# Kernel optimization log

Measured on AMD Instinct MI355X. Metric: run time of the kernel, lower is better.

Reference implementation:

```python
import jax, jax.numpy as jnp
import numpy as np

DIM = 768
HID = 1536
EPS = 1e-12
SCALE = float(np.sqrt(DIM))


def _layernorm(x, gamma, beta):
    mu = jnp.mean(x, axis=-1, keepdims=True)
    var = jnp.mean(jnp.square(x - mu), axis=-1, keepdims=True)
    return (x - mu) * jax.lax.rsqrt(var + EPS) * gamma + beta


def setup_inputs() -> dict:
    key = jax.random.key(0)
    ks = jax.random.split(key, 16)
    s = 1.0 / np.sqrt(DIM)
    sh = 1.0 / np.sqrt(HID)
    x = jax.random.normal(ks[0], (8, 2048, DIM), dtype=jnp.float32)
    return {
        "x": x,
        "Wq": jax.random.uniform(ks[1], (DIM, DIM), jnp.float32, -s, s),
        "bq": jax.random.uniform(ks[2], (DIM,), jnp.float32, -s, s),
        "Wk": jax.random.uniform(ks[3], (DIM, DIM), jnp.float32, -s, s),
        "bk": jax.random.uniform(ks[4], (DIM,), jnp.float32, -s, s),
        "Wv": jax.random.uniform(ks[5], (DIM, DIM), jnp.float32, -s, s),
        "bv": jax.random.uniform(ks[6], (DIM,), jnp.float32, -s, s),
        "Wp": jax.random.uniform(ks[7], (DIM, DIM), jnp.float32, -s, s),
        "bp": jax.random.uniform(ks[8], (DIM,), jnp.float32, -s, s),
        "g1": jnp.ones((DIM,), jnp.float32),
        "be1": jnp.zeros((DIM,), jnp.float32),
        "W1": jax.random.uniform(ks[9], (HID, DIM), jnp.float32, -s, s),
        "b1": jax.random.uniform(ks[10], (HID,), jnp.float32, -s, s),
        "W2": jax.random.uniform(ks[11], (DIM, HID), jnp.float32, -sh, sh),
        "b2": jax.random.uniform(ks[12], (DIM,), jnp.float32, -sh, sh),
        "g2": jnp.ones((DIM,), jnp.float32),
        "be2": jnp.zeros((DIM,), jnp.float32),
    }


def reference(x, Wq, bq, Wk, bk, Wv, bv, Wp, bp, g1, be1, W1, b1, W2, b2, g2, be2):
    # NOTE: original code does NOT split into heads; single full-dim bmm attention.
    Q = jnp.einsum("bsd,ed->bse", x, Wq) + bq  # [B,S,D]
    K = jnp.einsum("bsd,ed->bse", x, Wk) + bk
    V = jnp.einsum("bsd,ed->bse", x, Wv) + bv
    alpha = jnp.einsum("bqd,bkd->bqk", Q, K) / SCALE  # [B,S,S]
    alpha = jax.nn.softmax(alpha, axis=-1)
    attn = jnp.einsum("bqk,bkd->bqd", alpha, V)
    attn = jnp.einsum("bsd,ed->bse", attn, Wp) + bp  # linear_proj
    h = _layernorm(x + attn, g1, be1)
    mlp = jax.nn.gelu(jnp.einsum("bsd,hd->bsh", h, W1) + b1, approximate=False)
    mlp = jnp.einsum("bsh,dh->bsd", mlp, W2) + b2
    return _layernorm(h + mlp, g2, be2)
```

## Files before the change

kernel.cpp:

```cpp
#include <hip/hip_runtime.h>
#include <math.h>

#define D_MODEL 768
#define D_HID   1536
#define N_BATCH 8
#define SEQLEN  2048
#define NROWS   (N_BATCH*SEQLEN)

typedef unsigned short u16;
typedef unsigned char  u8;
typedef __attribute__((ext_vector_type(8))) short bfrag;
typedef __attribute__((ext_vector_type(4))) float facc;

__device__ __forceinline__ u16 f2bf(float f) {
  unsigned u = __float_as_uint(f);
  u += 0x7fffu + ((u >> 16) & 1u);
  return (u16)(u >> 16);
}
__device__ __forceinline__ float bf2f(u16 u) {
  return __uint_as_float((unsigned)u << 16);
}
__device__ __forceinline__ u8 f2fp8(float f) {
  return (u8)(__builtin_amdgcn_cvt_pk_fp8_f32(f, f, 0, 0) & 0xff);
}

__device__ __forceinline__ void async16(const void* g, void* l) {
  __builtin_amdgcn_global_load_lds((const __attribute__((address_space(1))) void*)g,
                                   (__attribute__((address_space(3))) void*)l,
                                   16, 0, 0);
}
__device__ __forceinline__ void wg_barrier() {
  asm volatile("" ::: "memory");
  __builtin_amdgcn_s_barrier();
  asm volatile("" ::: "memory");
}
#define VMCNT(n) asm volatile("s_waitcnt vmcnt(" #n ")" ::: "memory")

__global__ __launch_bounds__(256) void cvt_all(
    const float* __restrict__ x,  const float* __restrict__ Wq,
    const float* __restrict__ Wk, const float* __restrict__ Wv,
    const float* __restrict__ Wp, const float* __restrict__ W1,
    const float* __restrict__ W2, const float* __restrict__ bq,
    const float* __restrict__ bk, const float* __restrict__ bv,
    u16* __restrict__ XB, u16* __restrict__ WQKV, u16* __restrict__ WPB,
    u16* __restrict__ W1B, u16* __restrict__ W2B, float* __restrict__ BQKV,
    float* __restrict__ LSUM) {
  long i = (long)blockIdx.x * 256 + threadIdx.x;
  const float* src; u16* dst; long off;
  if      (i < 3145728) { src = x;  dst = XB;             off = i; }
  else if (i < 3293184) { src = Wq; dst = WQKV;           off = i - 3145728; }
  else if (i < 3440640) { src = Wk; dst = WQKV + 589824;  off = i - 3293184; }
  else if (i < 3588096) { src = Wv; dst = WQKV + 1179648; off = i - 3440640; }
  else if (i < 3735552) { src = Wp; dst = WPB;            off = i - 3588096; }
  else if (i < 4030464) { src = W1; dst = W1B;            off = i - 3735552; }
  else if (i < 4325376) { src = W2; dst = W2B;            off = i - 4030464; }
  else if (i < 4325952) {
    long j = i - 4325376;
    const float* s = (j < 192) ? bq : (j < 384) ? bk : bv;
    long o = (j < 192) ? j : (j < 384) ? j - 192 : j - 384;
    ((float4*)BQKV)[j] = ((const float4*)s)[o];
    return;
  } else if (i < 4330048) {
    float4 zz = {0.f, 0.f, 0.f, 0.f};
    ((float4*)LSUM)[i - 4325952] = zz;
    return;
  } else return;
  float4 v = ((const float4*)src)[off];
  ushort4 o4;
  o4.x = f2bf(v.x); o4.y = f2bf(v.y); o4.z = f2bf(v.z); o4.w = f2bf(v.w);
  *reinterpret_cast<ushort4*>(dst + off * 4) = o4;
}

enum { EPI_EXP = 1, EPI_DIV = 2, EPI_GELU = 4, EPI_QKV = 5, EPI_RES = 6 };

template<int EPI>
__global__ __launch_bounds__(256, 3)
void gemm_bt(const u16* __restrict__ Aall, const u16* __restrict__ Ball,
             void* __restrict__ Cout,
             int M, int N, int K,
             long sA, long sB, long sC,
             const float* __restrict__ bias,
             const u16* __restrict__ resid,
             float* __restrict__ lsum,
             float scale)
{
  __shared__ __align__(16) char smem[49152];
  const int z = blockIdx.z;
  const u16* A = Aall + (long)z * sA;
  const u16* B = Ball + (long)z * sB;
  const int bm = blockIdx.x, bn = blockIdx.y;
  const int tid = (int)threadIdx.x;
  const int lane = tid & 63, wv = tid >> 6;
  const int wr = wv >> 1, wc = wv & 1;

  facc acc[4][4] = {};

  const int srow2 = tid >> 2;
  const int c4 = tid & 3;
  const int skey = (srow2 >> 1) & 3;
  const int sc = ((c4 ^ skey) << 3);
  const u16* Abase = A + (long)(bm * 128) * K;
  const u16* Bbase = B + (long)(bn * 128) * K;
  const int fr = lane & 15, g0 = lane >> 4;
  const int rkey = (fr >> 1) & 3;
  const int nt = K >> 5;

  auto STAGE = [&](int t, int b) {
    char* Asb = smem + b * 16384;
    char* Bsb = Asb + 8192;
    const long k0 = (long)t << 5;
#pragma unroll
    for (int p = 0; p < 2; ++p) {
      async16(Abase + (long)(p * 64 + srow2) * K + k0 + sc, Asb + p * 4096 + tid * 16);
      async16(Bbase + (long)(p * 64 + srow2) * K + k0 + sc, Bsb + p * 4096 + tid * 16);
    }
  };

  STAGE(0, 0); STAGE(1, 1);
  int rb_ = 0, sb_ = 2;
  for (int t = 0; t < nt; ++t) {
    if (t < nt - 1) { VMCNT(4); } else { VMCNT(0); }
    wg_barrier();
    if (t + 2 < nt) STAGE(t + 2, sb_);
    const u16* As = (const u16*)(smem + rb_ * 16384);
    const u16* Bs = As + 4096;
    bfrag af[4], bf[4];
#pragma unroll
    for (int i = 0; i < 4; ++i) {
      const int r = wr * 64 + i * 16 + fr;
      af[i] = *(const bfrag*)(As + r * 32 + ((g0 ^ rkey) << 3));
    }
#pragma unroll
    for (int j = 0; j < 4; ++j) {
      const int r = wc * 64 + j * 16 + fr;
      bf[j] = *(const bfrag*)(Bs + r * 32 + ((g0 ^ rkey) << 3));
    }
    __builtin_amdgcn_s_setprio(1);
#pragma unroll
    for (int i = 0; i < 4; ++i)
#pragma unroll
      for (int j = 0; j < 4; ++j)
        acc[i][j] = __builtin_amdgcn_mfma_f32_16x16x32_bf16(af[i], bf[j], acc[i][j], 0, 0, 0);
    __builtin_amdgcn_s_setprio(0);
    rb_ = (rb_ == 2) ? 0 : rb_ + 1;
    sb_ = (sb_ == 2) ? 0 : sb_ + 1;
  }
  wg_barrier();

  const int rb = bm * 128 + wr * 64;
  const int cb = bn * 128 + wc * 64;
  const int quad = lane >> 4;

  if constexpr (EPI == EPI_QKV) {
    const int c64 = bn * 2 + wc;
    const int which = c64 / 12;
    float bj[4];
#pragma unroll
    for (int j = 0; j < 4; ++j) bj[j] = bias[cb + j * 16 + fr];
    if (which == 2) {
      u8* VT_ = (u8*)resid;
      const int zb = rb >> 11;
      const int seqb = (rb & 2047) + quad * 4;
      const int dimb = (c64 - 24) * 64;
#pragma unroll
      for (int i = 0; i < 4; ++i) {
#pragma unroll
        for (int j = 0; j < 4; ++j) {
          const int dim = dimb + j * 16 + fr;
          unsigned v01 = __builtin_amdgcn_cvt_pk_fp8_f32(acc[i][j][0] + bj[j],
                                                         acc[i][j][1] + bj[j], 0, 0);
          unsigned v23 = __builtin_amdgcn_cvt_pk_fp8_f32(acc[i][j][2] + bj[j],
                                                         acc[i][j][3] + bj[j], 0, 0);
          unsigned w = (v01 & 0xffffu) | (v23 << 16);
          *reinterpret_cast<unsigned*>(VT_ + (long)zb * D_MODEL * SEQLEN +
                                       (long)dim * SEQLEN + seqb + i * 16) = w;
        }
      }
      return;
    }
    u8* ep8 = (u8*)(smem + wv * 8192);
    u8* Cg = (u8*)Cout + (long)which * NROWS * D_MODEL;
    const int cbo = (c64 - which * 12) * 64;
#pragma unroll
    for (int i = 0; i < 4; ++i)
#pragma unroll
      for (int r = 0; r < 4; ++r) {
        const int lrow = i * 16 + quad * 4 + r;
#pragma unroll
        for (int j = 0; j < 4; ++j)
          ep8[lrow * 64 + j * 16 + fr] = f2fp8(acc[i][j][r] + bj[j]);
      }
#pragma unroll
    for (int it = 0; it < 4; ++it) {
      const int lr = it * 16 + (lane >> 2);
      const int ch = (lane & 3) << 4;
      int4 d = *(const int4*)(ep8 + lr * 64 + ch);
      *reinterpret_cast<int4*>(Cg + (long)(rb + lr) * D_MODEL + cbo + ch) = d;
    }
  } else if constexpr (EPI == EPI_GELU) {
    u16* ep16 = (u16*)(smem + wv * 8192);
    u16* Cg = (u16*)Cout + (long)z * sC;
    float bj[4];
#pragma unroll
    for (int j = 0; j < 4; ++j) bj[j] = bias[cb + j * 16 + fr];
#pragma unroll
    for (int i = 0; i < 4; ++i) {
#pragma unroll
      for (int r = 0; r < 4; ++r) {
        const int lrow = i * 16 + quad * 4 + r;
#pragma unroll
        for (int j = 0; j < 4; ++j) {
          float t = acc[i][j][r] + bj[j];
          float y = 0.7978845608f * (t + 0.044715f * t * t * t);
          float e = __expf(-2.f * fabsf(y));
          float th = (1.f - e) / (1.f + e);
          th = (y < 0.f) ? -th : th;
          ep16[lrow * 64 + j * 16 + fr] = f2bf(0.5f * t * (1.f + th));
        }
      }
    }
#pragma unroll
    for (int it = 0; it < 8; ++it) {
      const int lr = it * 8 + (lane >> 3);
      const int ch = (lane & 7) << 3;
      int4 d = *(const int4*)(ep16 + lr * 64 + ch);
      *reinterpret_cast<int4*>(Cg + (long)(rb + lr) * N + cb + ch) = d;
    }
  } else {
    float* ep32 = (float*)(smem + wv * 8192);
    u16* Cg = (u16*)Cout;
#pragma unroll
    for (int h = 0; h < 2; ++h) {
#pragma unroll
      for (int i2 = 0; i2 < 2; ++i2) {
        const int i = h * 2 + i2;
#pragma unroll
        for (int r = 0; r < 4; ++r) {
          const int lrow = i2 * 16 + quad * 4 + r;
#pragma unroll
          for (int j = 0; j < 4; ++j)
            ep32[lrow * 64 + j * 16 + fr] = acc[i][j][r];
        }
      }
#pragma unroll
      for (int it = 0; it < 8; ++it) {
        const int lr = it * 4 + (lane >> 4);
        const int ch = (lane & 15) << 2;
        float4 d = *(const float4*)(ep32 + lr * 64 + ch);
        const int row = rb + h * 32 + lr;
        const int gcol = cb + ch;
        const long gi = (long)row * N + gcol;
        ushort4 rv = *(const ushort4*)(resid + gi);
        float4 bb = *(const float4*)(bias + gcol);
        ushort4 o;
        o.x = f2bf(d.x + bb.x + bf2f(rv.x));
        o.y = f2bf(d.y + bb.y + bf2f(rv.y));
        o.z = f2bf(d.z + bb.z + bf2f(rv.z));
        o.w = f2bf(d.w + bb.w + bf2f(rv.w));
        *reinterpret_cast<ushort4*>(Cg + gi) = o;
      }
      wg_barrier();
    }
  }
  (void)lsum; (void)scale; (void)M;
}

template<int EPI>
__global__ __launch_bounds__(256, 3)
void gemm_f8(const u8* __restrict__ Aall, const u8* __restrict__ Ball,
             void* __restrict__ Cout,
             int M, int N, int K,
             long sA, long sB, long sC,
             float* __restrict__ lsum, float scale)
{
  __shared__ __align__(16) char smem[49152];
  const int z = blockIdx.z;
  const u8* A = Aall + (long)z * sA;
  const u8* B = Ball + (long)z * sB;
  const int bm = blockIdx.x, bn = blockIdx.y;
  const int tid = (int)threadIdx.x;
  const int lane = tid & 63, wv = tid >> 6;
  const int wr = wv >> 1, wc = wv & 1;

  facc acc[4][4] = {};

  const int srow2 = tid >> 2;
  const int c4 = tid & 3;
  const int skey = (srow2 >> 1) & 3;
  const int scb = ((c4 ^ skey) << 4);
  const u8* Abase = A + (long)(bm * 128) * K;
  const u8* Bbase = B + (long)(bn * 128) * K;
  const int fr = lane & 15, g0 = lane >> 4;
  const int rkey = (fr >> 1) & 3;
  const int nt = K >> 6;

  auto STAGE = [&](int t, int b) {
    char* Asb = smem + b * 16384;
    char* Bsb = Asb + 8192;
    const long k0 = (long)t << 6;
#pragma unroll
    for (int p = 0; p < 2; ++p) {
      async16(Abase + (long)(p * 64 + srow2) * K + k0 + scb, Asb + p * 4096 + tid * 16);
      async16(Bbase + (long)(p * 64 + srow2) * K + k0 + scb, Bsb + p * 4096 + tid * 16);
    }
  };

  STAGE(0, 0); STAGE(1, 1);
  int rb_ = 0, sb_ = 2;
  for (int t = 0; t < nt; ++t) {
    if (t < nt - 1) { VMCNT(4); } else { VMCNT(0); }
    wg_barrier();
    if (t + 2 < nt) STAGE(t + 2, sb_);
    const u8* As = (const u8*)(smem + rb_ * 16384);
    const u8* Bs = As + 8192;
#pragma unroll
    for (int s = 0; s < 2; ++s) {
      long af[4], bf[4];
      const int cc = (s * 2 + (g0 >> 1)) ^ rkey;
      const int h8 = (g0 & 1) << 3;
#pragma unroll
      for (int i = 0; i < 4; ++i) {
        const int r = wr * 64 + i * 16 + fr;
        af[i] = *(const long*)(As + r * 64 + (cc << 4) + h8);
      }
#pragma unroll
      for (int j = 0; j < 4; ++j) {
        const int r = wc * 64 + j * 16 + fr;
        bf[j] = *(const long*)(Bs + r * 64 + (cc << 4) + h8);
      }
      __builtin_amdgcn_s_setprio(1);
#pragma unroll
      for (int i = 0; i < 4; ++i)
#pragma unroll
        for (int j = 0; j < 4; ++j)
          acc[i][j] = __builtin_amdgcn_mfma_f32_16x16x32_fp8_fp8(af[i], bf[j], acc[i][j], 0, 0, 0);
      __builtin_amdgcn_s_setprio(0);
    }
    rb_ = (rb_ == 2) ? 0 : rb_ + 1;
    sb_ = (sb_ == 2) ? 0 : sb_ + 1;
  }
  wg_barrier();

  const int rb = bm * 128 + wr * 64;
  const int cb = bn * 128 + wc * 64;
  const int quad = lane >> 4;

  if constexpr (EPI == EPI_EXP) {
    u8* ep8 = (u8*)(smem + wv * 4096);
    u8* Cg = (u8*)Cout + (long)z * sC;
#pragma unroll
    for (int i = 0; i < 4; ++i) {
#pragma unroll
      for (int r = 0; r < 4; ++r) {
        const int lrow = i * 16 + quad * 4 + r;
        const int row = rb + lrow;
        float rs = 0.f;
#pragma unroll
        for (int j = 0; j < 4; ++j) {
          float e = __expf(acc[i][j][r] * scale - 3.0f);
          rs += e;
          ep8[lrow * 64 + j * 16 + fr] = f2fp8(e);
        }
        rs += __shfl_xor(rs, 1);
        rs += __shfl_xor(rs, 2);
        rs += __shfl_xor(rs, 4);
        rs += __shfl_xor(rs, 8);
        if (fr == 0) atomicAdd(&lsum[(long)z * M + row], rs);
      }
    }
#pragma unroll
    for (int it = 0; it < 4; ++it) {
      const int lr = it * 16 + (lane >> 2);
      const int ch = (lane & 3) << 4;
      int4 d = *(const int4*)(ep8 + lr * 64 + ch);
      *reinterpret_cast<int4*>(Cg + (long)(rb + lr) * N + cb + ch) = d;
    }
  } else {
    u16* ep16 = (u16*)(smem + wv * 4096);
    u16* Cg = (u16*)Cout + (long)z * sC;
#pragma unroll
    for (int h = 0; h < 2; ++h) {
#pragma unroll
      for (int i2 = 0; i2 < 2; ++i2) {
        const int i = h * 2 + i2;
#pragma unroll
        for (int r = 0; r < 4; ++r) {
          const int lrow = i2 * 16 + quad * 4 + r;
          const int row = rb + h * 32 + lrow;
          const float inv = 1.f / lsum[(long)z * M + row];
#pragma unroll
          for (int j = 0; j < 4; ++j)
            ep16[lrow * 64 + j * 16 + fr] = f2bf(acc[i][j][r] * inv);
        }
      }
#pragma unroll
      for (int it = 0; it < 4; ++it) {
        const int lr = it * 8 + (lane >> 3);
        const int ch = (lane & 7) << 3;
        int4 d = *(const int4*)(ep16 + lr * 64 + ch);
        *reinterpret_cast<int4*>(Cg + (long)(rb + h * 32 + lr) * N + cb + ch) = d;
      }
      wg_barrier();
    }
  }
}

__global__ __launch_bounds__(192) void layernorm_rows(const u16* __restrict__ in,
                                                      const float* __restrict__ gamma,
                                                      const float* __restrict__ beta,
                                                      float* __restrict__ outf,
                                                      u16* __restrict__ outb) {
  const int row = blockIdx.x;
  const int t = threadIdx.x;
  ushort4 uv = ((const ushort4*)(in + (long)row * D_MODEL))[t];
  float v0 = bf2f(uv.x), v1 = bf2f(uv.y), v2 = bf2f(uv.z), v3 = bf2f(uv.w);
  float s1 = v0 + v1 + v2 + v3;
  float s2 = v0 * v0 + v1 * v1 + v2 * v2 + v3 * v3;
#pragma unroll
  for (int o = 32; o; o >>= 1) { s1 += __shfl_xor(s1, o); s2 += __shfl_xor(s2, o); }
  __shared__ float r1[3], r2[3];
  const int wv = t >> 6, ln = t & 63;
  if (ln == 0) { r1[wv] = s1; r2[wv] = s2; }
  __syncthreads();
  s1 = r1[0] + r1[1] + r1[2];
  s2 = r2[0] + r2[1] + r2[2];
  const float mu = s1 * (1.f / 768.f);
  const float var = s2 * (1.f / 768.f) - mu * mu;
  const float rstd = rsqrtf(var + 1e-12f);
  float4 gv = ((const float4*)gamma)[t];
  float4 bv = ((const float4*)beta)[t];
  float o0 = (v0 - mu) * rstd * gv.x + bv.x;
  float o1 = (v1 - mu) * rstd * gv.y + bv.y;
  float o2 = (v2 - mu) * rstd * gv.z + bv.z;
  float o3 = (v3 - mu) * rstd * gv.w + bv.w;
  if (outf) {
    float4 ov = {o0, o1, o2, o3};
    ((float4*)(outf + (long)row * D_MODEL))[t] = ov;
  }
  if (outb) {
    ushort4 ob;
    ob.x = f2bf(o0); ob.y = f2bf(o1); ob.z = f2bf(o2); ob.w = f2bf(o3);
    ((ushort4*)(outb + (long)row * D_MODEL))[t] = ob;
  }
}

static const size_t OFF_WP   = 0;
static const size_t OFF_W1   = 1179648;
static const size_t OFF_W2   = 3538944;
static const size_t OFF_LSUM = 5898240;
static const size_t OFF_BQKV = 5963776;
static const size_t OFF_QB   = 6291456;
static const size_t OFF_KB   = 18874368;
static const size_t OFF_VT   = 31457280;
static const size_t OFF_EB   = 44040192;
static const size_t OFF_CTX  = 77594624;
static const size_t OFF_XB   = 102760448;
static const size_t OFF_WQKV = 127926272;
static const size_t OFF_M1B  = 131465216;

extern "C" void kernel_launch(void* const* d_in, const int* in_sizes, int n_in,
                              void* d_out, int out_size, void* d_ws, size_t ws_size,
                              hipStream_t stream) {
  const float* x   = (const float*)d_in[0];
  const float* Wq  = (const float*)d_in[1];
  const float* bq  = (const float*)d_in[2];
  const float* Wk  = (const float*)d_in[3];
  const float* bk  = (const float*)d_in[4];
  const float* Wv  = (const float*)d_in[5];
  const float* bv  = (const float*)d_in[6];
  const float* Wp  = (const float*)d_in[7];
  const float* bp  = (const float*)d_in[8];
  const float* g1  = (const float*)d_in[9];
  const float* be1 = (const float*)d_in[10];
  const float* W1  = (const float*)d_in[11];
  const float* b1  = (const float*)d_in[12];
  const float* W2  = (const float*)d_in[13];
  const float* b2  = (const float*)d_in[14];
  const float* g2  = (const float*)d_in[15];
  const float* be2 = (const float*)d_in[16];

  char* ws = (char*)d_ws;
  u16*   WPB  = (u16*)(ws + OFF_WP);
  u16*   W1B  = (u16*)(ws + OFF_W1);
  u16*   W2B  = (u16*)(ws + OFF_W2);
  float* LSUM = (float*)(ws + OFF_LSUM);
  float* BQKV = (float*)(ws + OFF_BQKV);
  u8*    QB   = (u8*)(ws + OFF_QB);
  u8*    KB   = (u8*)(ws + OFF_KB);
  u8*    VT   = (u8*)(ws + OFF_VT);
  u8*    EB   = (u8*)(ws + OFF_EB);
  u16*   CTX  = (u16*)(ws + OFF_CTX);
  u16*   XB   = (u16*)(ws + OFF_XB);
  u16*   WQKV = (u16*)(ws + OFF_WQKV);
  u16*   M1B  = (u16*)(ws + OFF_M1B);
  u16*   PB   = (u16*)(ws + OFF_QB);
  u16*   HB   = (u16*)(ws + OFF_EB);
  u16*   M2B  = (u16*)(ws + OFF_CTX);

  dim3 blk(256), blkl(192);

  cvt_all<<<dim3(16915), blk, 0, stream>>>(x, Wq, Wk, Wv, Wp, W1, W2, bq, bk, bv,
                                           XB, WQKV, WPB, W1B, W2B, BQKV, LSUM);

  gemm_bt<EPI_QKV><<<dim3(128, 18, 1), blk, 0, stream>>>(XB, WQKV, QB,
      NROWS, 3 * D_MODEL, D_MODEL, 0, 0, 0, BQKV, (const u16*)VT, nullptr, 0.f);

  const float sc = 1.0f / sqrtf((float)D_MODEL);
  gemm_f8<EPI_EXP><<<dim3(16, 16, 8), blk, 0, stream>>>(QB, KB, EB,
      SEQLEN, SEQLEN, D_MODEL,
      (long)SEQLEN * D_MODEL, (long)SEQLEN * D_MODEL, (long)SEQLEN * SEQLEN,
      LSUM, sc);
  gemm_f8<EPI_DIV><<<dim3(16, 6, 8), blk, 0, stream>>>(EB, VT, CTX,
      SEQLEN, D_MODEL, SEQLEN,
      (long)SEQLEN * SEQLEN, (long)D_MODEL * SEQLEN, (long)SEQLEN * D_MODEL,
      LSUM, 0.f);
  gemm_bt<EPI_RES><<<dim3(128, 6, 1), blk, 0, stream>>>(CTX, WPB, PB,
      NROWS, D_MODEL, D_MODEL, 0, 0, 0, bp, XB, nullptr, 0.f);
  layernorm_rows<<<dim3(NROWS), blkl, 0, stream>>>(PB, g1, be1, nullptr, HB);
  gemm_bt<EPI_GELU><<<dim3(128, 12, 1), blk, 0, stream>>>(HB, W1B, M1B,
      NROWS, D_HID, D_MODEL, 0, 0, 0, b1, nullptr, nullptr, 0.f);
  gemm_bt<EPI_RES><<<dim3(128, 6, 1), blk, 0, stream>>>(M1B, W2B, M2B,
      NROWS, D_MODEL, D_HID, 0, 0, 0, b2, HB, nullptr, 0.f);
  layernorm_rows<<<dim3(NROWS), blkl, 0, stream>>>(M2B, g2, be2, (float*)d_out, nullptr);

  (void)in_sizes; (void)n_in; (void)out_size; (void)ws_size;
}
```

Baseline: 466.7 us.

## Widen bf16 GEMM tiles to 128x256, double-buffer QK GEMM, drop lsum atomics

The bf16 GEMMs now run 512-thread blocks with 128x256 tiles, so each A tile is reused across twice as many columns and fewer blocks are launched. The fp8 QK^T GEMM gets a templated pipeline depth (double-buffered, with a higher occupancy bound), while the PV GEMM keeps the triple-buffered loop. Softmax row sums are no longer accumulated with atomicAdd. Each wave writes a partial into a 32-slot-per-row buffer, and the divide epilogue reduces those slots with shuffles. In exchange the change brings larger LDS use, lower occupancy for the bf16 GEMMs, and a scratch buffer for the sums that reuses the M1B region.

Result: faster. 450.1 us (-3.6%).

```diff
diff --git a/kernel.cpp b/kernel.cpp
--- a/kernel.cpp
+++ b/kernel.cpp
@@ -74,24 +74,22 @@
 enum { EPI_EXP = 1, EPI_DIV = 2, EPI_GELU = 4, EPI_QKV = 5, EPI_RES = 6 };
 
 template<int EPI>
-__global__ __launch_bounds__(256, 3)
-void gemm_bt(const u16* __restrict__ Aall, const u16* __restrict__ Ball,
-             void* __restrict__ Cout,
-             int M, int N, int K,
-             long sA, long sB, long sC,
-             const float* __restrict__ bias,
-             const u16* __restrict__ resid,
-             float* __restrict__ lsum,
-             float scale)
+__global__ __launch_bounds__(512, 2)
+void gemm_bt512(const u16* __restrict__ Aall, const u16* __restrict__ Ball,
+                void* __restrict__ Cout,
+                int M, int N, int K,
+                long sA, long sB, long sC,
+                const float* __restrict__ bias,
+                const u16* __restrict__ resid,
+                float* __restrict__ lsum, float scale)
 {
-  __shared__ __align__(16) char smem[49152];
-  const int z = blockIdx.z;
-  const u16* A = Aall + (long)z * sA;
-  const u16* B = Ball + (long)z * sB;
+  __shared__ __align__(16) char smem[73728];
+  const u16* A = Aall;
+  const u16* B = Ball;
   const int bm = blockIdx.x, bn = blockIdx.y;
   const int tid = (int)threadIdx.x;
   const int lane = tid & 63, wv = tid >> 6;
-  const int wr = wv >> 1, wc = wv & 1;
+  const int wr = wv >> 2, wc = wv & 3;
 
   facc acc[4][4] = {};
 
@@ -100,29 +98,28 @@
   const int skey = (srow2 >> 1) & 3;
   const int sc = ((c4 ^ skey) << 3);
   const u16* Abase = A + (long)(bm * 128) * K;
-  const u16* Bbase = B + (long)(bn * 128) * K;
+  const u16* Bbase = B + (long)(bn * 256) * K;
   const int fr = lane & 15, g0 = lane >> 4;
   const int rkey = (fr >> 1) & 3;
   const int nt = K >> 5;
 
   auto STAGE = [&](int t, int b) {
-    char* Asb = smem + b * 16384;
+    char* Asb = smem + b * 24576;
     char* Bsb = Asb + 8192;
     const long k0 = (long)t << 5;
-#pragma unroll
-    for (int p = 0; p < 2; ++p) {
-      async16(Abase + (long)(p * 64 + srow2) * K + k0 + sc, Asb + p * 4096 + tid * 16);
-      async16(Bbase + (long)(p * 64 + srow2) * K + k0 + sc, Bsb + p * 4096 + tid * 16);
-    }
+    async16(Abase + (long)srow2 * K + k0 + sc, Asb + tid * 16);
+#pragma unroll
+    for (int p = 0; p < 2; ++p)
+      async16(Bbase + (long)(p * 128 + srow2) * K + k0 + sc, Bsb + p * 8192 + tid * 16);
   };
 
   STAGE(0, 0); STAGE(1, 1);
   int rb_ = 0, sb_ = 2;
   for (int t = 0; t < nt; ++t) {
-    if (t < nt - 1) { VMCNT(4); } else { VMCNT(0); }
+    if (t < nt - 1) { VMCNT(3); } else { VMCNT(0); }
     wg_barrier();
     if (t + 2 < nt) STAGE(t + 2, sb_);
-    const u16* As = (const u16*)(smem + rb_ * 16384);
+    const u16* As = (const u16*)(smem + rb_ * 24576);
     const u16* Bs = As + 4096;
     bfrag af[4], bf[4];
 #pragma unroll
@@ -148,11 +145,11 @@
   wg_barrier();
 
   const int rb = bm * 128 + wr * 64;
-  const int cb = bn * 128 + wc * 64;
+  const int cb = bn * 256 + wc * 64;
   const int quad = lane >> 4;
 
   if constexpr (EPI == EPI_QKV) {
-    const int c64 = bn * 2 + wc;
+    const int c64 = bn * 4 + wc;
     const int which = c64 / 12;
     float bj[4];
 #pragma unroll
@@ -199,7 +196,7 @@
     }
   } else if constexpr (EPI == EPI_GELU) {
     u16* ep16 = (u16*)(smem + wv * 8192);
-    u16* Cg = (u16*)Cout + (long)z * sC;
+    u16* Cg = (u16*)Cout;
     float bj[4];
 #pragma unroll
     for (int j = 0; j < 4; ++j) bj[j] = bias[cb + j * 16 + fr];
@@ -259,21 +256,20 @@
         o.w = f2bf(d.w + bb.w + bf2f(rv.w));
         *reinterpret_cast<ushort4*>(Cg + gi) = o;
       }
-      wg_barrier();
     }
   }
-  (void)lsum; (void)scale; (void)M;
-}
-
-template<int EPI>
-__global__ __launch_bounds__(256, 3)
+  (void)lsum; (void)scale; (void)M; (void)sA; (void)sB; (void)sC;
+}
+
+template<int EPI, int DEPTH>
+__global__ __launch_bounds__(256, 6 - DEPTH)
 void gemm_f8(const u8* __restrict__ Aall, const u8* __restrict__ Ball,
              void* __restrict__ Cout,
              int M, int N, int K,
              long sA, long sB, long sC,
              float* __restrict__ lsum, float scale)
 {
-  __shared__ __align__(16) char smem[49152];
+  __shared__ __align__(16) char smem[DEPTH * 16384];
   const int z = blockIdx.z;
   const u8* A = Aall + (long)z * sA;
   const u8* B = Ball + (long)z * sB;
@@ -305,13 +301,8 @@
     }
   };
 
-  STAGE(0, 0); STAGE(1, 1);
-  int rb_ = 0, sb_ = 2;
-  for (int t = 0; t < nt; ++t) {
-    if (t < nt - 1) { VMCNT(4); } else { VMCNT(0); }
-    wg_barrier();
-    if (t + 2 < nt) STAGE(t + 2, sb_);
-    const u8* As = (const u8*)(smem + rb_ * 16384);
+  auto COMPUTE = [&](int buf) {
+    const u8* As = (const u8*)(smem + buf * 16384);
     const u8* Bs = As + 8192;
 #pragma unroll
     for (int s = 0; s < 2; ++s) {
@@ -336,10 +327,30 @@
           acc[i][j] = __builtin_amdgcn_mfma_f32_16x16x32_fp8_fp8(af[i], bf[j], acc[i][j], 0, 0, 0);
       __builtin_amdgcn_s_setprio(0);
     }
-    rb_ = (rb_ == 2) ? 0 : rb_ + 1;
-    sb_ = (sb_ == 2) ? 0 : sb_ + 1;
+  };
+
+  if constexpr (DEPTH == 3) {
+    STAGE(0, 0); STAGE(1, 1);
+    int rb_ = 0, sb_ = 2;
+    for (int t = 0; t < nt; ++t) {
+      if (t < nt - 1) { VMCNT(4); } else { VMCNT(0); }
+      wg_barrier();
+      if (t + 2 < nt) STAGE(t + 2, sb_);
+      COMPUTE(rb_);
+      rb_ = (rb_ == 2) ? 0 : rb_ + 1;
+      sb_ = (sb_ == 2) ? 0 : sb_ + 1;
+    }
+    wg_barrier();
+  } else {
+    STAGE(0, 0); STAGE(1, 1);
+    for (int t = 0; t < nt; ++t) {
+      if (t < nt - 1) { VMCNT(4); } else { VMCNT(0); }
+      wg_barrier();
+      COMPUTE(t & 1);
+      wg_barrier();
+      if (t + 2 < nt) STAGE(t + 2, t & 1);
+    }
   }
-  wg_barrier();
 
   const int rb = bm * 128 + wr * 64;
   const int cb = bn * 128 + wc * 64;
@@ -365,7 +376,8 @@
         rs += __shfl_xor(rs, 2);
         rs += __shfl_xor(rs, 4);
         rs += __shfl_xor(rs, 8);
-        if (fr == 0) atomicAdd(&lsum[(long)z * M + row], rs);
+        if (fr == 0)
+          lsum[(((long)z * M + row) << 5) + (bn << 1) + wc] = rs;
       }
     }
 #pragma unroll
@@ -387,7 +399,14 @@
         for (int r = 0; r < 4; ++r) {
           const int lrow = i2 * 16 + quad * 4 + r;
           const int row = rb + h * 32 + lrow;
-          const float inv = 1.f / lsum[(long)z * M + row];
+          const float2 p2 = *reinterpret_cast<const float2*>(
+              lsum + (((long)z * M + row) << 5) + (fr << 1));
+          float ls = p2.x + p2.y;
+          ls += __shfl_xor(ls, 1);
+          ls += __shfl_xor(ls, 2);
+          ls += __shfl_xor(ls, 4);
+          ls += __shfl_xor(ls, 8);
+          const float inv = 1.f / ls;
 #pragma unroll
           for (int j = 0; j < 4; ++j)
             ep16[lrow * 64 + j * 16 + fr] = f2bf(acc[i][j][r] * inv);
@@ -496,30 +515,31 @@
   u16*   PB   = (u16*)(ws + OFF_QB);
   u16*   HB   = (u16*)(ws + OFF_EB);
   u16*   M2B  = (u16*)(ws + OFF_CTX);
-
-  dim3 blk(256), blkl(192);
+  float* LS32 = (float*)(ws + OFF_M1B);
+
+  dim3 blk(256), blkg(512), blkl(192);
 
   cvt_all<<<dim3(16915), blk, 0, stream>>>(x, Wq, Wk, Wv, Wp, W1, W2, bq, bk, bv,
                                            XB, WQKV, WPB, W1B, W2B, BQKV, LSUM);
 
-  gemm_bt<EPI_QKV><<<dim3(128, 18, 1), blk, 0, stream>>>(XB, WQKV, QB,
+  gemm_bt512<EPI_QKV><<<dim3(128, 9, 1), blkg, 0, stream>>>(XB, WQKV, QB,
       NROWS, 3 * D_MODEL, D_MODEL, 0, 0, 0, BQKV, (const u16*)VT, nullptr, 0.f);
 
   const float sc = 1.0f / sqrtf((float)D_MODEL);
-  gemm_f8<EPI_EXP><<<dim3(16, 16, 8), blk, 0, stream>>>(QB, KB, EB,
+  gemm_f8<EPI_EXP, 2><<<dim3(16, 16, 8), blk, 0, stream>>>(QB, KB, EB,
       SEQLEN, SEQLEN, D_MODEL,
       (long)SEQLEN * D_MODEL, (long)SEQLEN * D_MODEL, (long)SEQLEN * SEQLEN,
-      LSUM, sc);
-  gemm_f8<EPI_DIV><<<dim3(16, 6, 8), blk, 0, stream>>>(EB, VT, CTX,
+      LS32, sc);
+  gemm_f8<EPI_DIV, 3><<<dim3(16, 6, 8), blk, 0, stream>>>(EB, VT, CTX,
       SEQLEN, D_MODEL, SEQLEN,
       (long)SEQLEN * SEQLEN, (long)D_MODEL * SEQLEN, (long)SEQLEN * D_MODEL,
-      LSUM, 0.f);
-  gemm_bt<EPI_RES><<<dim3(128, 6, 1), blk, 0, stream>>>(CTX, WPB, PB,
+      LS32, 0.f);
+  gemm_bt512<EPI_RES><<<dim3(128, 3, 1), blkg, 0, stream>>>(CTX, WPB, PB,
       NROWS, D_MODEL, D_MODEL, 0, 0, 0, bp, XB, nullptr, 0.f);
   layernorm_rows<<<dim3(NROWS), blkl, 0, stream>>>(PB, g1, be1, nullptr, HB);
-  gemm_bt<EPI_GELU><<<dim3(128, 12, 1), blk, 0, stream>>>(HB, W1B, M1B,
+  gemm_bt512<EPI_GELU><<<dim3(128, 6, 1), blkg, 0, stream>>>(HB, W1B, M1B,
       NROWS, D_HID, D_MODEL, 0, 0, 0, b1, nullptr, nullptr, 0.f);
-  gemm_bt<EPI_RES><<<dim3(128, 6, 1), blk, 0, stream>>>(M1B, W2B, M2B,
+  gemm_bt512<EPI_RES><<<dim3(128, 3, 1), blkg, 0, stream>>>(M1B, W2B, M2B,
       NROWS, D_MODEL, D_HID, 0, 0, 0, b2, HB, nullptr, 0.f);
   layernorm_rows<<<dim3(NROWS), blkl, 0, stream>>>(M2B, g2, be2, (float*)d_out, nullptr);
 
```
